# Kernel tuning notes

Hardware: AMD Instinct MI355X
Metric: run time of the kernel (lower is better)

The kernel has to match this reference:

```python
import jax, jax.numpy as jnp
import numpy as np

THRESH = 1.0
GAMA = 1.0
TAU0 = 0.5

# ZIF surrogate spike: forward hard step, backward triangular surrogate
@jax.custom_vjp
def zif(x):
    return (x > 0).astype(x.dtype)

def _zif_fwd(x):
    return zif(x), x

def _zif_bwd(x, g):
    surr = (1.0 / GAMA) * (1.0 / GAMA) * jnp.clip(GAMA - jnp.abs(x), 0.0, None)
    return (g * surr,)

zif.defvjp(_zif_fwd, _zif_bwd)


def setup_inputs() -> dict:
    key = jax.random.key(0)
    k1, k2, k3, k4, k5 = jax.random.split(key, 5)
    B, T, C, H, W = 32, 8, 128, 32, 32
    red = 4
    x = jax.random.normal(k1, (B, T, C, H, W), dtype=jnp.float32)
    # fc1: Linear(C, C//red); fc2: Linear(C//red, 1); PyTorch default init scale
    s1 = 1.0 / np.sqrt(C)
    s2 = 1.0 / np.sqrt(C // red)
    w1 = jax.random.uniform(k2, (C // red, C), jnp.float32, -s1, s1)
    b1 = jax.random.uniform(k3, (C // red,), jnp.float32, -s1, s1)
    w2 = jax.random.uniform(k4, (1, C // red), jnp.float32, -s2, s2)
    b2 = jax.random.uniform(k5, (1,), jnp.float32, -s2, s2)
    return {"x": x, "w1": w1, "b1": b1, "w2": w2, "b2": b2}


def reference(x, w1, b1, w2, b2):
    B, T, C, H, W = x.shape

    def step(carry, xt):
        mem, tau = carry  # mem: [B,C,H,W], tau: [B,1,1,1]
        mem = mem * tau + xt
        # SE-style gating MLP on channel means
        x_mean = jnp.mean(mem, axis=(-1, -2))          # [B,C]
        embed = jax.nn.relu(x_mean @ w1.T + b1)        # [B,C//r]
        lifp = jax.nn.sigmoid(embed @ w2.T + b2)       # [B,1]
        new_tau = lifp[:, :, None, None]               # [B,1,1,1]
        spike = zif(mem - THRESH)
        mem = (1.0 - spike) * mem
        return (mem, new_tau), spike

    mem0 = jnp.zeros((B, C, H, W), dtype=x.dtype)
    tau0 = jnp.full((B, 1, 1, 1), TAU0, dtype=x.dtype)
    xt = jnp.transpose(x, (1, 0, 2, 3, 4))  # [T,B,C,H,W]
    _, spikes = jax.lax.scan(step, (mem0, tau0), xt)
    return jnp.transpose(spikes, (1, 0, 2, 3, 4))  # [B,T,C,H,W]
```

## Files before the change

kernel.cpp:

```cpp
#include <hip/hip_runtime.h>

typedef float v4f __attribute__((ext_vector_type(4)));

#define NB   32
#define NT   8
#define NC   128
#define NQ   256
#define CRED 32

#define NWORDS (NT * NB * NC * 2)

__device__ unsigned long long g_xw[NWORDS];

__global__ __launch_bounds__(256)
void lif_init() {
    int i = threadIdx.x + blockIdx.x * blockDim.x;
    if (i < NWORDS) g_xw[i] = 0ull;
}

#define LDS_BARRIER() asm volatile("s_waitcnt lgkmcnt(0)\n\ts_barrier" ::: "memory")

__global__ __launch_bounds__(256, 4)
void dynamic_lif(const float* __restrict__ x,
                 const float* __restrict__ w1,
                 const float* __restrict__ b1,
                 const float* __restrict__ w2,
                 const float* __restrict__ b2,
                 float* __restrict__ out)
{
    const int bid = blockIdx.x;
    const int b   = bid >> 5;
    const int c0  = (bid & 31) << 2;
    const int tid = threadIdx.x;
    const int wv  = tid >> 6;
    const int ln  = tid & 63;

    __shared__ double       s_part[4][4];
    __shared__ unsigned int s_w[256];
    __shared__ float        s_tau;

    const v4f* __restrict__ x4 = (const v4f*)x;
    v4f* __restrict__ o4       = (v4f*)out;

    v4f mem[4];
    #pragma unroll
    for (int p = 0; p < 4; ++p) mem[p] = (v4f){0.f, 0.f, 0.f, 0.f};

    float tau = 0.5f;

    v4f xv[4];
    #pragma unroll
    for (int p = 0; p < 4; ++p)
        xv[p] = __builtin_nontemporal_load(x4 + ((b * NT + 0) * NC + c0 + p) * NQ + tid);

    for (int t = 0; t < NT; ++t) {
        double psum[4];
        #pragma unroll
        for (int p = 0; p < 4; ++p) {
            v4f m = mem[p];
            m.x = fmaf(m.x, tau, xv[p].x);
            m.y = fmaf(m.y, tau, xv[p].y);
            m.z = fmaf(m.z, tau, xv[p].z);
            m.w = fmaf(m.w, tau, xv[p].w);
            psum[p] = ((double)m.x + (double)m.y) + ((double)m.z + (double)m.w);
            mem[p] = m;
        }

        #pragma unroll
        for (int p = 0; p < 4; ++p) {
            double s = psum[p];
            #pragma unroll
            for (int off = 32; off > 0; off >>= 1) s += __shfl_down(s, off);
            if (ln == 0) s_part[p][wv] = s;
        }
        LDS_BARRIER();

        if (t < NT - 1 && tid < 4) {
            double s = (s_part[tid][0] + s_part[tid][1]) +
                       (s_part[tid][2] + s_part[tid][3]);
            double mean = s * (1.0 / 1024.0);
            unsigned long long bits = __double_as_longlong(mean);
            unsigned long long tag  = ((unsigned long long)(t + 1)) << 32;
            const int base = ((t * NB + b) * NC + c0 + tid) * 2;
            __hip_atomic_store(&g_xw[base + 0], tag | (bits & 0xffffffffull),
                               __ATOMIC_RELAXED, __HIP_MEMORY_SCOPE_AGENT);
            __hip_atomic_store(&g_xw[base + 1], tag | (bits >> 32),
                               __ATOMIC_RELAXED, __HIP_MEMORY_SCOPE_AGENT);
        }

        if (t + 1 < NT) {
            #pragma unroll
            for (int p = 0; p < 4; ++p)
                xv[p] = __builtin_nontemporal_load(
                    x4 + ((b * NT + (t + 1)) * NC + c0 + p) * NQ + tid);
        }
        #pragma unroll
        for (int p = 0; p < 4; ++p) {
            v4f m = mem[p];
            v4f sp;
            sp.x = (m.x > 1.0f) ? 1.0f : 0.0f;
            sp.y = (m.y > 1.0f) ? 1.0f : 0.0f;
            sp.z = (m.z > 1.0f) ? 1.0f : 0.0f;
            sp.w = (m.w > 1.0f) ? 1.0f : 0.0f;
            __builtin_nontemporal_store(sp, o4 + ((b * NT + t) * NC + c0 + p) * NQ + tid);
            m.x = (m.x > 1.0f) ? 0.0f : m.x;
            m.y = (m.y > 1.0f) ? 0.0f : m.y;
            m.z = (m.z > 1.0f) ? 0.0f : m.z;
            m.w = (m.w > 1.0f) ? 0.0f : m.w;
            mem[p] = m;
        }

        if (t == NT - 1) break;

        {
            const int idx = ((t * NB + b) * NC + (tid >> 1)) * 2 + (tid & 1);
            const unsigned int want = (unsigned int)(t + 1);
            unsigned long long w;
            for (;;) {
                w = __hip_atomic_load(&g_xw[idx], __ATOMIC_RELAXED,
                                      __HIP_MEMORY_SCOPE_AGENT);
                if ((unsigned int)(w >> 32) == want) break;
                __builtin_amdgcn_s_sleep(1);
            }
            s_w[tid] = (unsigned int)w;
        }
        LDS_BARRIER();

        double e = 0.0;
        if (tid < CRED) {
            const v4f* __restrict__ w1v = (const v4f*)(w1 + tid * NC);
            double acc = (double)b1[tid];
            #pragma unroll
            for (int q = 0; q < NC / 4; ++q) {
                v4f wq = w1v[q];
                #pragma unroll
                for (int k = 0; k < 4; ++k) {
                    const int c = 4 * q + k;
                    unsigned long long bits =
                        ((unsigned long long)s_w[2 * c + 1] << 32) | s_w[2 * c];
                    double xm = __longlong_as_double(bits);
                    acc += xm * (double)((k == 0) ? wq.x : (k == 1) ? wq.y
                                         : (k == 2) ? wq.z : wq.w);
                }
            }
            double emb = acc > 0.0 ? acc : 0.0;
            e = emb * (double)w2[tid];
        }
        #pragma unroll
        for (int off = 32; off > 0; off >>= 1) e += __shfl_down(e, off);
        if (tid == 0) {
            double z = e + (double)b2[0];
            s_tau = (float)(1.0 / (1.0 + exp(-z)));
        }
        LDS_BARRIER();
        tau = s_tau;
    }
}

extern "C" void kernel_launch(void* const* d_in, const int* in_sizes, int n_in,
                              void* d_out, int out_size, void* d_ws, size_t ws_size,
                              hipStream_t stream) {
    const float* x  = (const float*)d_in[0];
    const float* w1 = (const float*)d_in[1];
    const float* b1 = (const float*)d_in[2];
    const float* w2 = (const float*)d_in[3];
    const float* b2 = (const float*)d_in[4];
    float* out      = (float*)d_out;

    hipLaunchKernelGGL(lif_init, dim3((NWORDS + 255) / 256), dim3(256),
                       0, stream);
    hipLaunchKernelGGL(dynamic_lif, dim3(NB * NC / 4), dim3(256), 0, stream,
                       x, w1, b1, w2, b2, out);
}
```

Baseline: 265.8 us.

## Confine cross-block mean polling and gating MLP to wave 0, dropping a barrier

Wave 0 alone now publishes the channel means, polls the global exchange buffer for all 128 channel means (four loads per lane), and computes the gating MLP and tau. It relies on an intra-wave lgkmcnt wait instead of a block-wide barrier between the polling and the MLP. The other waves only prefetch the next x slice and store spikes, so one block-wide barrier per timestep is removed and the remaining waves are not held up by the poll. The cost is a longer serial critical path inside wave 0, and the correctness of s_w now depends on wave-level LDS ordering.

```diff
diff --git a/kernel.cpp b/kernel.cpp
--- a/kernel.cpp
+++ b/kernel.cpp
@@ -75,83 +75,122 @@
         }
         LDS_BARRIER();
 
-        if (t < NT - 1 && tid < 4) {
-            double s = (s_part[tid][0] + s_part[tid][1]) +
-                       (s_part[tid][2] + s_part[tid][3]);
-            double mean = s * (1.0 / 1024.0);
-            unsigned long long bits = __double_as_longlong(mean);
-            unsigned long long tag  = ((unsigned long long)(t + 1)) << 32;
-            const int base = ((t * NB + b) * NC + c0 + tid) * 2;
-            __hip_atomic_store(&g_xw[base + 0], tag | (bits & 0xffffffffull),
-                               __ATOMIC_RELAXED, __HIP_MEMORY_SCOPE_AGENT);
-            __hip_atomic_store(&g_xw[base + 1], tag | (bits >> 32),
-                               __ATOMIC_RELAXED, __HIP_MEMORY_SCOPE_AGENT);
-        }
-
-        if (t + 1 < NT) {
+        if (t == NT - 1) {
+            #pragma unroll
+            for (int p = 0; p < 4; ++p) {
+                v4f m = mem[p];
+                v4f sp;
+                sp.x = (m.x > 1.0f) ? 1.0f : 0.0f;
+                sp.y = (m.y > 1.0f) ? 1.0f : 0.0f;
+                sp.z = (m.z > 1.0f) ? 1.0f : 0.0f;
+                sp.w = (m.w > 1.0f) ? 1.0f : 0.0f;
+                __builtin_nontemporal_store(sp,
+                    o4 + ((b * NT + t) * NC + c0 + p) * NQ + tid);
+            }
+            break;
+        }
+
+        if (wv == 0) {
+            if (ln < 4) {
+                double s = (s_part[ln][0] + s_part[ln][1]) +
+                           (s_part[ln][2] + s_part[ln][3]);
+                double mean = s * (1.0 / 1024.0);
+                unsigned long long bits = __double_as_longlong(mean);
+                unsigned long long tag  = ((unsigned long long)(t + 1)) << 32;
+                const int base = ((t * NB + b) * NC + c0 + ln) * 2;
+                __hip_atomic_store(&g_xw[base + 0], tag | (bits & 0xffffffffull),
+                                   __ATOMIC_RELAXED, __HIP_MEMORY_SCOPE_AGENT);
+                __hip_atomic_store(&g_xw[base + 1], tag | (bits >> 32),
+                                   __ATOMIC_RELAXED, __HIP_MEMORY_SCOPE_AGENT);
+            }
             #pragma unroll
             for (int p = 0; p < 4; ++p)
                 xv[p] = __builtin_nontemporal_load(
                     x4 + ((b * NT + (t + 1)) * NC + c0 + p) * NQ + tid);
-        }
-        #pragma unroll
-        for (int p = 0; p < 4; ++p) {
-            v4f m = mem[p];
-            v4f sp;
-            sp.x = (m.x > 1.0f) ? 1.0f : 0.0f;
-            sp.y = (m.y > 1.0f) ? 1.0f : 0.0f;
-            sp.z = (m.z > 1.0f) ? 1.0f : 0.0f;
-            sp.w = (m.w > 1.0f) ? 1.0f : 0.0f;
-            __builtin_nontemporal_store(sp, o4 + ((b * NT + t) * NC + c0 + p) * NQ + tid);
-            m.x = (m.x > 1.0f) ? 0.0f : m.x;
-            m.y = (m.y > 1.0f) ? 0.0f : m.y;
-            m.z = (m.z > 1.0f) ? 0.0f : m.z;
-            m.w = (m.w > 1.0f) ? 0.0f : m.w;
-            mem[p] = m;
-        }
-
-        if (t == NT - 1) break;
-
-        {
-            const int idx = ((t * NB + b) * NC + (tid >> 1)) * 2 + (tid & 1);
-            const unsigned int want = (unsigned int)(t + 1);
-            unsigned long long w;
-            for (;;) {
-                w = __hip_atomic_load(&g_xw[idx], __ATOMIC_RELAXED,
-                                      __HIP_MEMORY_SCOPE_AGENT);
-                if ((unsigned int)(w >> 32) == want) break;
-                __builtin_amdgcn_s_sleep(1);
-            }
-            s_w[tid] = (unsigned int)w;
-        }
-        LDS_BARRIER();
-
-        double e = 0.0;
-        if (tid < CRED) {
-            const v4f* __restrict__ w1v = (const v4f*)(w1 + tid * NC);
-            double acc = (double)b1[tid];
-            #pragma unroll
-            for (int q = 0; q < NC / 4; ++q) {
-                v4f wq = w1v[q];
+            #pragma unroll
+            for (int p = 0; p < 4; ++p) {
+                v4f m = mem[p];
+                v4f sp;
+                sp.x = (m.x > 1.0f) ? 1.0f : 0.0f;
+                sp.y = (m.y > 1.0f) ? 1.0f : 0.0f;
+                sp.z = (m.z > 1.0f) ? 1.0f : 0.0f;
+                sp.w = (m.w > 1.0f) ? 1.0f : 0.0f;
+                __builtin_nontemporal_store(sp,
+                    o4 + ((b * NT + t) * NC + c0 + p) * NQ + tid);
+                m.x = (m.x > 1.0f) ? 0.0f : m.x;
+                m.y = (m.y > 1.0f) ? 0.0f : m.y;
+                m.z = (m.z > 1.0f) ? 0.0f : m.z;
+                m.w = (m.w > 1.0f) ? 0.0f : m.w;
+                mem[p] = m;
+            }
+
+            {
+                const int wbase = (t * NB + b) * NC * 2;
+                const unsigned int want = (unsigned int)(t + 1);
                 #pragma unroll
-                for (int k = 0; k < 4; ++k) {
-                    const int c = 4 * q + k;
-                    unsigned long long bits =
-                        ((unsigned long long)s_w[2 * c + 1] << 32) | s_w[2 * c];
-                    double xm = __longlong_as_double(bits);
-                    acc += xm * (double)((k == 0) ? wq.x : (k == 1) ? wq.y
-                                         : (k == 2) ? wq.z : wq.w);
+                for (int j = 0; j < 4; ++j) {
+                    unsigned long long w;
+                    for (;;) {
+                        w = __hip_atomic_load(&g_xw[wbase + ln + 64 * j],
+                                              __ATOMIC_RELAXED,
+                                              __HIP_MEMORY_SCOPE_AGENT);
+                        if ((unsigned int)(w >> 32) == want) break;
+                        __builtin_amdgcn_s_sleep(1);
+                    }
+                    s_w[ln + 64 * j] = (unsigned int)w;
                 }
             }
-            double emb = acc > 0.0 ? acc : 0.0;
-            e = emb * (double)w2[tid];
-        }
-        #pragma unroll
-        for (int off = 32; off > 0; off >>= 1) e += __shfl_down(e, off);
-        if (tid == 0) {
-            double z = e + (double)b2[0];
-            s_tau = (float)(1.0 / (1.0 + exp(-z)));
-        }
+            asm volatile("s_waitcnt lgkmcnt(0)" ::: "memory");
+
+            double e = 0.0;
+            if (ln < CRED) {
+                const v4f* __restrict__ w1v = (const v4f*)(w1 + ln * NC);
+                double acc = (double)b1[ln];
+                #pragma unroll
+                for (int q = 0; q < NC / 4; ++q) {
+                    v4f wq = w1v[q];
+                    #pragma unroll
+                    for (int k = 0; k < 4; ++k) {
+                        const int c = 4 * q + k;
+                        unsigned long long bits =
+                            ((unsigned long long)s_w[2 * c + 1] << 32) | s_w[2 * c];
+                        double xm = __longlong_as_double(bits);
+                        acc += xm * (double)((k == 0) ? wq.x : (k == 1) ? wq.y
+                                             : (k == 2) ? wq.z : wq.w);
+                    }
+                }
+                double emb = acc > 0.0 ? acc : 0.0;
+                e = emb * (double)w2[ln];
+            }
+            #pragma unroll
+            for (int off = 32; off > 0; off >>= 1) e += __shfl_down(e, off);
+            if (ln == 0) {
+                double z = e + (double)b2[0];
+                s_tau = (float)(1.0 / (1.0 + exp(-z)));
+            }
+        } else {
+            #pragma unroll
+            for (int p = 0; p < 4; ++p)
+                xv[p] = __builtin_nontemporal_load(
+                    x4 + ((b * NT + (t + 1)) * NC + c0 + p) * NQ + tid);
+            #pragma unroll
+            for (int p = 0; p < 4; ++p) {
+                v4f m = mem[p];
+                v4f sp;
+                sp.x = (m.x > 1.0f) ? 1.0f : 0.0f;
+                sp.y = (m.y > 1.0f) ? 1.0f : 0.0f;
+                sp.z = (m.z > 1.0f) ? 1.0f : 0.0f;
+                sp.w = (m.w > 1.0f) ? 1.0f : 0.0f;
+                __builtin_nontemporal_store(sp,
+                    o4 + ((b * NT + t) * NC + c0 + p) * NQ + tid);
+                m.x = (m.x > 1.0f) ? 0.0f : m.x;
+                m.y = (m.y > 1.0f) ? 0.0f : m.y;
+                m.z = (m.z > 1.0f) ? 0.0f : m.z;
+                m.w = (m.w > 1.0f) ? 0.0f : m.w;
+                mem[p] = m;
+            }
+        }
+
         LDS_BARRIER();
         tau = s_tau;
     }
```

New measurement: 271.4 us. 2.1% more time.
